# Performance work log

Measured on AMD Instinct MI355X. Metric: run time of the kernel, lower is better.

The kernel has to match this reference:

```python
import jax, jax.numpy as jnp
import numpy as np

B, T, NN, GP, D, H = 16, 12, 325, 64, 512, 8
HD = D // H
N_TOT = GP + NN  # 389


def setup_inputs() -> dict:
    key = jax.random.key(0)
    ks = jax.random.split(key, 16)
    def lin_w(k, fan_in, fan_out):
        return jax.random.normal(k, (fan_in, fan_out), jnp.float32) * np.float32(1.0 / np.sqrt(fan_in))
    d = {"X": jax.random.normal(ks[0], (B, T, N_TOT, D), jnp.float32)}
    i = 1
    for p in ("e", "d"):
        for w in ("q", "k", "v", "o"):
            d[f"{p}_w{w}"] = lin_w(ks[i], D, D); i += 1
            d[f"{p}_b{w}"] = jnp.zeros((D,), jnp.float32)
    d["ff_w1"] = lin_w(ks[i], D, 4 * D); i += 1
    d["ff_b1"] = jnp.zeros((4 * D,), jnp.float32)
    d["ff_w2"] = lin_w(ks[i], 4 * D, D); i += 1
    d["ff_b2"] = jnp.zeros((D,), jnp.float32)
    d["ln1_g"] = jnp.ones((D,), jnp.float32)
    d["ln1_b"] = jnp.zeros((D,), jnp.float32)
    d["ln2_g"] = jnp.ones((D,), jnp.float32)
    d["ln2_b"] = jnp.zeros((D,), jnp.float32)
    return d


def _mha(q, k, v, wq, bq, wk, bk, wv, bv, wo, bo):
    # torch split(head_dim,-1)+cat(0) == reshape last dim to (H, HD)
    Q = (q @ wq + bq).reshape(q.shape[:-1] + (H, HD))
    K = (k @ wk + bk).reshape(k.shape[:-1] + (H, HD))
    V = (v @ wv + bv).reshape(v.shape[:-1] + (H, HD))
    s = jnp.einsum('btqhd,btkhd->bthqk', Q, K) * np.float32(1.0 / np.sqrt(HD))
    a = jax.nn.softmax(s, axis=-1)  # dropout=0.0 -> identity
    o = jnp.einsum('bthqk,btkhd->btqhd', a, V).reshape(q.shape)
    return o @ wo + bo


def _ln(x, g, b):
    m = x.mean(-1, keepdims=True)
    v = x.var(-1, keepdims=True)
    return (x - m) * jax.lax.rsqrt(v + 1e-5) * g + b


def reference(X, e_wq, e_bq, e_wk, e_bk, e_wv, e_bv, e_wo, e_bo,
              d_wq, d_bq, d_wk, d_bk, d_wv, d_bv, d_wo, d_bo,
              ff_w1, ff_b1, ff_w2, ff_b2, ln1_g, ln1_b, ln2_g, ln2_b):
    glob = X[:, :, :GP, :]   # global patch queries
    patch = X[:, :, GP:, :]  # last num_nodes tokens (== x[:,:,-patch_len:])
    # eattn: global queries attend to node tokens
    t = _mha(glob, patch, patch, e_wq, e_bq, e_wk, e_bk, e_wv, e_bv, e_wo, e_bo)
    # in-place write x[:,:,:global_patch] = t -> K/V for dattn is [t, patch]
    x_kv = jnp.concatenate([t, patch], axis=2)
    # dattn: node queries attend to full (updated) sequence
    out = _mha(patch, x_kv, x_kv, d_wq, d_bq, d_wk, d_bk, d_wv, d_bv, d_wo, d_bo)
    out = _ln(patch + out, ln1_g, ln1_b)  # residual is original node tokens
    ff = jax.nn.relu(out @ ff_w1 + ff_b1) @ ff_w2 + ff_b2
    out = _ln(out + ff, ln2_g, ln2_b)
    return jnp.concatenate([t, out], axis=2)
```

## Files before the change

kernel.cpp:

```cpp
#include <hip/hip_runtime.h>

typedef unsigned short u16;
typedef __attribute__((ext_vector_type(4))) float f32x4;
typedef __attribute__((ext_vector_type(8))) __bf16 bf16x8;
typedef __attribute__((ext_vector_type(4))) unsigned short u16x4;
typedef __attribute__((ext_vector_type(8))) unsigned short u16x8;

#define DEV static __device__ __forceinline__
#define MFMA_B16 __builtin_amdgcn_mfma_f32_16x16x32_bf16


DEV u16 f2b(float f) {
  union { float f; unsigned u; } c; c.f = f;
  return (u16)((c.u + 0x7FFFu + ((c.u >> 16) & 1u)) >> 16);
}

DEV void async_cp16(void* lds, const void* g) {
  __builtin_amdgcn_global_load_lds((__attribute__((address_space(1))) void*)g,
                                   (__attribute__((address_space(3))) void*)lds,
                                   16, 0, 0);
}

__global__ __launch_bounds__(256) void transpose_w(const float* __restrict__ W,
                                                   u16* __restrict__ Wt,
                                                   int K, int N) {
  __shared__ float t[32][33];
  const int n0 = blockIdx.x * 32, k0 = blockIdx.y * 32;
  const int tx = threadIdx.x, ty = threadIdx.y;
  for (int i = ty; i < 32; i += 8) t[i][tx] = W[(size_t)(k0 + i) * N + n0 + tx];
  __syncthreads();
  for (int i = ty; i < 32; i += 8)
    Wt[(size_t)(n0 + i) * K + k0 + tx] = f2b(t[tx][i]);
}

__global__ __launch_bounds__(256) void convert_x(const float* __restrict__ X,
                                                 u16* __restrict__ Xg,
                                                 u16* __restrict__ Xp) {
  const size_t i = ((size_t)blockIdx.x * 256 + threadIdx.x) * 4;
  const f32x4 v = *(const f32x4*)(X + i);
  const size_t row = i >> 9;
  const int col = (int)(i & 511);
  const int bt = (int)(row / 389), n = (int)(row - (size_t)bt * 389);
  u16x4 w;
#pragma unroll
  for (int u = 0; u < 4; u++) w[u] = f2b(v[u]);
  u16* dst = (n < 64) ? (Xg + (((size_t)bt * 64 + n) << 9) + col)
                      : (Xp + (((size_t)bt * 328 + (n - 64)) << 9) + col);
  *(u16x4*)dst = w;
}

template <int MODE>
__global__ __launch_bounds__(256) void gemm_bt(
    const u16* __restrict__ A, const u16* __restrict__ Bt,
    const float* __restrict__ bias, float* outF, u16* outB,
    int M, int N, int K, int rows_per, int row_ofs, int aux) {
  __shared__ u16 SH[2][128 * 64];
  u16* As = &SH[0][0];
  u16* Bs = &SH[1][0];
  const int tid = threadIdx.x;
  const int lane = tid & 63, wid = tid >> 6;
  const int l4 = lane >> 4, l16 = lane & 15;
  const int n0 = blockIdx.x * 128, m0 = blockIdx.y * 128;
  const int wr = (wid >> 1) * 64, wc = (wid & 1) * 64;

  const int srow = lane >> 3;
  const int scol = 8 * ((lane & 7) ^ srow);
  const u16* gA = A + (size_t)(m0 + wid * 32 + srow) * K + scol;
  const u16* gB = Bt + (size_t)(n0 + wid * 32 + srow) * K + scol;

  f32x4 acc[4][4] = {};

  for (int kk = 0; kk < K; kk += 64) {
    if (kk) __syncthreads();
#pragma unroll
    for (int c = 0; c < 4; c++) {
      async_cp16(As + (wid * 32 + c * 8) * 64, gA + (size_t)(c * 8) * K + kk);
      async_cp16(Bs + (wid * 32 + c * 8) * 64, gB + (size_t)(c * 8) * K + kk);
    }
    __syncthreads();
#pragma unroll
    for (int hh = 0; hh < 2; hh++) {
      const int sw = (((hh * 64 + l4 * 16) ^ ((l16 & 7) << 4)) >> 1);
      bf16x8 af[4], bfr[4];
#pragma unroll
      for (int i = 0; i < 4; i++)
        af[i] = *(const bf16x8*)(As + (wr + i * 16 + l16) * 64 + sw);
#pragma unroll
      for (int j = 0; j < 4; j++)
        bfr[j] = *(const bf16x8*)(Bs + (wc + j * 16 + l16) * 64 + sw);
#pragma unroll
      for (int i = 0; i < 4; i++)
#pragma unroll
        for (int j = 0; j < 4; j++)
          acc[i][j] = MFMA_B16(af[i], bfr[j], acc[i][j], 0, 0, 0);
    }
  }

  if constexpr (MODE == 6) {
    __syncthreads();
    u16* cs = &SH[0][0];
#pragma unroll
    for (int j = 0; j < 4; j++) {
      const float bv = bias[n0 + wc + j * 16 + l16];
#pragma unroll
      for (int i = 0; i < 4; i++)
#pragma unroll
        for (int r = 0; r < 4; r++)
          cs[(wr + i * 16 + l4 * 4 + r) * 128 + wc + j * 16 + l16] =
              f2b(acc[i][j][r] + bv);
    }
    __syncthreads();
    const int c = tid & 127;
    const int kvh = (tid >> 7) * 64;
    const int gh = (n0 + c) >> 6, gd = (n0 + c) & 63;
#pragma unroll
    for (int g = 0; g < 8; g++) {
      const int row0 = m0 + kvh + g * 8;
      if (row0 >= M) break;
      const int bt0 = row0 / rows_per;
      const int rr = row0 - bt0 * rows_per;
      u16x8 w;
#pragma unroll
      for (int e = 0; e < 8; e++) w[e] = cs[(kvh + g * 8 + e) * 128 + c];
      *(u16x8*)(outB + (((size_t)bt0 * 8 + gh) * 64 + gd) * (size_t)aux +
                row_ofs + rr) = w;
    }
  } else {
#pragma unroll
    for (int j = 0; j < 4; j++) {
      const int col = n0 + wc + j * 16 + l16;
      const float bv = bias[col];
#pragma unroll
      for (int i = 0; i < 4; i++) {
#pragma unroll
        for (int r = 0; r < 4; r++) {
          const int row = m0 + wr + i * 16 + l4 * 4 + r;
          if (row >= M) continue;
          const float v = acc[i][j][r] + bv;
          if constexpr (MODE == 0) {
            outB[(size_t)row * N + col] = f2b(v);
          } else if constexpr (MODE == 1) {
            const int bt = row / rows_per, rr = row - bt * rows_per;
            if (rr < aux)
              outB[((size_t)bt * 389 + row_ofs + rr) * 512 + col] = f2b(v);
          } else if constexpr (MODE == 2) {
            const int bt = row >> 6, rr = row & 63;
            outF[((size_t)bt * 389 + rr) * 512 + col] = v;
            outB[(size_t)row * 512 + col] = f2b(v);
          } else if constexpr (MODE == 3) {
            outF[(size_t)row * N + col] = v;
          } else if constexpr (MODE == 4) {
            outB[(size_t)row * N + col] = f2b(v > 0.f ? v : 0.f);
          } else {
            outF[(size_t)row * N + col] += v;
          }
        }
      }
    }
  }
}

template <int QS, int MQ, int KS, int NK, int NKP, bool T2>
__global__ __launch_bounds__(256) void attn_fused(
    const u16* __restrict__ Q, const u16* __restrict__ Kb,
    const u16* __restrict__ Vt, u16* __restrict__ O) {
  constexpr int NCH = NKP / 64;
  constexpr int QTW = T2 ? 128 : 64;
  constexpr int QP = (MQ + QTW - 1) / QTW;
  constexpr int PSTR = 72;
  __shared__ __align__(16) u16 Pl[4][2][16 * PSTR];
  const int tid = threadIdx.x, lane = tid & 63, wid = tid >> 6;
  const int l4 = lane >> 4, l16 = lane & 15;
  const int bt = blockIdx.x >> 3, h = blockIdx.x & 7;
  u16* pw0 = &Pl[wid][0][0];
  u16* pw1 = &Pl[wid][1][0];
  const u16* vb = Vt + ((size_t)bt * 8 + h) * (size_t)(64 * NKP);
  const u16* qb = Q + (size_t)bt * QS * 512 + h * 64;
  const u16* kb = Kb + (size_t)bt * KS * 512 + h * 64;

  for (int qp = 0; qp < QP; ++qp) {
    const int q0 = qp * QTW + wid * 16;
    const bool bL = T2 && (q0 + 64 < MQ);
    const u16* qpA = qb + (size_t)(q0 + l16) * 512 + l4 * 8;
    const bf16x8 aq0A = *(const bf16x8*)qpA;
    const bf16x8 aq1A = *(const bf16x8*)(qpA + 32);
    bf16x8 aq0B, aq1B;
    if (bL) {
      aq0B = *(const bf16x8*)(qpA + 32768);
      aq1B = *(const bf16x8*)(qpA + 32768 + 32);
    }

    f32x4 m0v, m1v, sum0, sum1, o0[4], o1[4];
#pragma unroll
    for (int r = 0; r < 4; r++) {
      m0v[r] = -1e30f; m1v[r] = -1e30f; sum0[r] = 0.f; sum1[r] = 0.f;
    }
#pragma unroll
    for (int j = 0; j < 4; j++) {
      o0[j] = (f32x4){0.f, 0.f, 0.f, 0.f};
      o1[j] = (f32x4){0.f, 0.f, 0.f, 0.f};
    }

    for (int ch = 0; ch < NCH; ++ch) {
      const int k0 = ch * 64;
      f32x4 sc0[4], sc1[4];
#pragma unroll
      for (int s = 0; s < 4; s++) {
        const u16* kp = kb + (size_t)(k0 + s * 16 + l16) * 512 + l4 * 8;
        const bf16x8 kf0 = *(const bf16x8*)kp;
        const bf16x8 kf1 = *(const bf16x8*)(kp + 32);
        f32x4 a = (f32x4){0.f, 0.f, 0.f, 0.f};
        a = MFMA_B16(aq0A, kf0, a, 0, 0, 0);
        a = MFMA_B16(aq1A, kf1, a, 0, 0, 0);
        sc0[s] = a;
        if (bL) {
          f32x4 bacc = (f32x4){0.f, 0.f, 0.f, 0.f};
          bacc = MFMA_B16(aq0B, kf0, bacc, 0, 0, 0);
          bacc = MFMA_B16(aq1B, kf1, bacc, 0, 0, 0);
          sc1[s] = bacc;
        }
      }
#pragma unroll
      for (int s = 0; s < 4; s++) {
        const bool vld = (k0 + s * 16 + l16) < NK;
#pragma unroll
        for (int r = 0; r < 4; r++) {
          sc0[s][r] = vld ? sc0[s][r] * 0.125f : -1e30f;
          if (bL) sc1[s][r] = vld ? sc1[s][r] * 0.125f : -1e30f;
        }
      }
      f32x4 c0, c1;
#pragma unroll
      for (int r = 0; r < 4; r++) {
        c0[r] = fmaxf(fmaxf(sc0[0][r], sc0[1][r]), fmaxf(sc0[2][r], sc0[3][r]));
        if (bL)
          c1[r] = fmaxf(fmaxf(sc1[0][r], sc1[1][r]), fmaxf(sc1[2][r], sc1[3][r]));
      }
#pragma unroll
      for (int mk = 1; mk < 16; mk <<= 1)
#pragma unroll
        for (int r = 0; r < 4; r++) {
          c0[r] = fmaxf(c0[r], __shfl_xor(c0[r], mk));
          if (bL) c1[r] = fmaxf(c1[r], __shfl_xor(c1[r], mk));
        }
      float g = c0[0] - m0v[0];
#pragma unroll
      for (int r = 1; r < 4; r++) g = fmaxf(g, c0[r] - m0v[r]);
      if (bL)
#pragma unroll
        for (int r = 0; r < 4; r++) g = fmaxf(g, c1[r] - m1v[r]);
      if (__any(g > 0.f)) {
#pragma unroll
        for (int r = 0; r < 4; r++) {
          float mn = fmaxf(m0v[r], c0[r]);
          float f = __expf(m0v[r] - mn);
          m0v[r] = mn; sum0[r] *= f;
#pragma unroll
          for (int j = 0; j < 4; j++) o0[j][r] *= f;
          if (bL) {
            mn = fmaxf(m1v[r], c1[r]); f = __expf(m1v[r] - mn);
            m1v[r] = mn; sum1[r] *= f;
#pragma unroll
            for (int j = 0; j < 4; j++) o1[j][r] *= f;
          }
        }
      }
#pragma unroll
      for (int s = 0; s < 4; s++)
#pragma unroll
        for (int r = 0; r < 4; r++) {
          const float e0 = __expf(sc0[s][r] - m0v[r]);
          sum0[r] += e0;
          pw0[(l4 * 4 + r) * PSTR + s * 16 + l16] = f2b(e0);
          if (bL) {
            const float e1 = __expf(sc1[s][r] - m1v[r]);
            sum1[r] += e1;
            pw1[(l4 * 4 + r) * PSTR + s * 16 + l16] = f2b(e1);
          }
        }
      asm volatile("s_waitcnt lgkmcnt(0)" ::: "memory");
      const bf16x8 apA0 = *(const bf16x8*)(pw0 + l16 * PSTR + l4 * 8);
      const bf16x8 apA1 = *(const bf16x8*)(pw0 + l16 * PSTR + 32 + l4 * 8);
      bf16x8 apB0, apB1;
      if (bL) {
        apB0 = *(const bf16x8*)(pw1 + l16 * PSTR + l4 * 8);
        apB1 = *(const bf16x8*)(pw1 + l16 * PSTR + 32 + l4 * 8);
      }
      __builtin_amdgcn_s_setprio(1);
#pragma unroll
      for (int j = 0; j < 4; j++) {
        const u16* vp = vb + (size_t)(j * 16 + l16) * NKP + k0 + l4 * 8;
        const bf16x8 v0 = *(const bf16x8*)vp;
        const bf16x8 v1 = *(const bf16x8*)(vp + 32);
        o0[j] = MFMA_B16(apA0, v0, o0[j], 0, 0, 0);
        o0[j] = MFMA_B16(apA1, v1, o0[j], 0, 0, 0);
        if (bL) {
          o1[j] = MFMA_B16(apB0, v0, o1[j], 0, 0, 0);
          o1[j] = MFMA_B16(apB1, v1, o1[j], 0, 0, 0);
        }
      }
      __builtin_amdgcn_s_setprio(0);
    }
#pragma unroll
    for (int mk = 1; mk < 16; mk <<= 1)
#pragma unroll
      for (int r = 0; r < 4; r++) {
        sum0[r] += __shfl_xor(sum0[r], mk);
        if (bL) sum1[r] += __shfl_xor(sum1[r], mk);
      }
#pragma unroll
    for (int j = 0; j < 4; j++)
#pragma unroll
      for (int r = 0; r < 4; r++) {
        const int qr = q0 + l4 * 4 + r;
        if (qr < MQ)
          O[((size_t)bt * QS + qr) * 512 + h * 64 + j * 16 + l16] =
              f2b(o0[j][r] / sum0[r]);
        if (bL && qr + 64 < MQ)
          O[((size_t)bt * QS + qr + 64) * 512 + h * 64 + j * 16 + l16] =
              f2b(o1[j][r] / sum1[r]);
      }
  }
}

__global__ __launch_bounds__(256) void ln_res(const float* __restrict__ X,
                                              float* __restrict__ y,
                                              const float* g, const float* b,
                                              u16* __restrict__ yb) {
  const int p = blockIdx.x * 4 + (threadIdx.x >> 6);
  const int lane = threadIdx.x & 63;
  const int bt = p / 325, n = p - bt * 325;
  const size_t yrow = ((size_t)bt * 328 + n) * 512;
  const float* xr = X + ((size_t)bt * 389 + 64 + n) * 512 + lane * 8;
  const float* ar = y + yrow + lane * 8;
  float vv[8];
  {
    const f32x4 a0 = *(const f32x4*)xr, a1 = *(const f32x4*)(xr + 4);
    const f32x4 b0 = *(const f32x4*)ar, b1 = *(const f32x4*)(ar + 4);
#pragma unroll
    for (int u = 0; u < 4; u++) { vv[u] = a0[u] + b0[u]; vv[u + 4] = a1[u] + b1[u]; }
  }
  float s1 = 0.f, s2 = 0.f;
#pragma unroll
  for (int u = 0; u < 8; u++) { s1 += vv[u]; s2 += vv[u] * vv[u]; }
  for (int m = 1; m < 64; m <<= 1) { s1 += __shfl_xor(s1, m); s2 += __shfl_xor(s2, m); }
  const float mean = s1 * (1.f / 512.f);
  const float inv = rsqrtf(s2 * (1.f / 512.f) - mean * mean + 1e-5f);
  const int c0 = lane * 8;
  f32x4 o0, o1;
  u16x8 ob;
#pragma unroll
  for (int u = 0; u < 8; u++) {
    const float o = (vv[u] - mean) * inv * g[c0 + u] + b[c0 + u];
    if (u < 4) o0[u] = o; else o1[u - 4] = o;
    ob[u] = f2b(o);
  }
  *(f32x4*)(y + yrow + c0) = o0;
  *(f32x4*)(y + yrow + c0 + 4) = o1;
  *(u16x8*)(yb + yrow + c0) = ob;
}

__global__ __launch_bounds__(256) void ln_out(const float* __restrict__ y,
                                              const float* g, const float* b,
                                              float* __restrict__ out) {
  const int p = blockIdx.x * 4 + (threadIdx.x >> 6);
  const int lane = threadIdx.x & 63;
  const int bt = p / 325, n = p - bt * 325;
  const float* yr = y + ((size_t)bt * 328 + n) * 512 + lane * 8;
  float vv[8];
  {
    const f32x4 a0 = *(const f32x4*)yr, a1 = *(const f32x4*)(yr + 4);
#pragma unroll
    for (int u = 0; u < 4; u++) { vv[u] = a0[u]; vv[u + 4] = a1[u]; }
  }
  float s1 = 0.f, s2 = 0.f;
#pragma unroll
  for (int u = 0; u < 8; u++) { s1 += vv[u]; s2 += vv[u] * vv[u]; }
  for (int m = 1; m < 64; m <<= 1) { s1 += __shfl_xor(s1, m); s2 += __shfl_xor(s2, m); }
  const float mean = s1 * (1.f / 512.f);
  const float inv = rsqrtf(s2 * (1.f / 512.f) - mean * mean + 1e-5f);
  const int c0 = lane * 8;
  f32x4 o0, o1;
#pragma unroll
  for (int u = 0; u < 8; u++) {
    const float o = (vv[u] - mean) * inv * g[c0 + u] + b[c0 + u];
    if (u < 4) o0[u] = o; else o1[u - 4] = o;
  }
  float* orow = out + ((size_t)bt * 389 + 64 + n) * 512 + c0;
  *(f32x4*)(orow) = o0;
  *(f32x4*)(orow + 4) = o1;
}

extern "C" void kernel_launch(void* const* d_in, const int* in_sizes, int n_in,
                              void* d_out, int out_size, void* d_ws,
                              size_t ws_size, hipStream_t stream) {
  (void)in_sizes; (void)n_in; (void)out_size; (void)ws_size;
  const float* X = (const float*)d_in[0];
  const float* W[8] = {(const float*)d_in[1],  (const float*)d_in[3],
                       (const float*)d_in[5],  (const float*)d_in[7],
                       (const float*)d_in[9],  (const float*)d_in[11],
                       (const float*)d_in[13], (const float*)d_in[15]};
  const float* Bv[8] = {(const float*)d_in[2],  (const float*)d_in[4],
                        (const float*)d_in[6],  (const float*)d_in[8],
                        (const float*)d_in[10], (const float*)d_in[12],
                        (const float*)d_in[14], (const float*)d_in[16]};
  const float* ff_w1 = (const float*)d_in[17];
  const float* ff_b1 = (const float*)d_in[18];
  const float* ff_w2 = (const float*)d_in[19];
  const float* ff_b2 = (const float*)d_in[20];
  const float* ln1_g = (const float*)d_in[21];
  const float* ln1_b = (const float*)d_in[22];
  const float* ln2_g = (const float*)d_in[23];
  const float* ln2_b = (const float*)d_in[24];
  float* out = (float*)d_out;
  char* ws = (char*)d_ws;

  constexpr size_t szW   = 8388608;
  constexpr size_t szXp  = (size_t)(62976 + 128) * 1024;
  constexpr size_t szQe  = (size_t)(12288 + 128) * 1024;
  constexpr size_t szKe  = szXp;
  constexpr size_t szVte = (size_t)192 * 8 * 64 * 384 * 2;
  constexpr size_t szKd  = (size_t)(74688 + 128) * 1024;
  constexpr size_t szVtd = (size_t)192 * 8 * 64 * 448 * 2;
  constexpr size_t o1 = szW;
  constexpr size_t o2 = o1 + szXp;
  constexpr size_t o3 = o2 + szQe;
  constexpr size_t o4 = o3 + szQe;
  constexpr size_t o5 = o4 + szQe + szKe + szVte;
  constexpr size_t o6 = o5 + szVtd;

  u16* wt     = (u16*)(ws);
  u16* Xp     = (u16*)(ws + o1);
  u16* yb     = (u16*)(ws + o1);
  u16* Xg     = (u16*)(ws + o2);
  u16* attn_e = (u16*)(ws + o2);
  u16* tb     = (u16*)(ws + o3);
  u16* Qe     = (u16*)(ws + o4);
  u16* Ke     = (u16*)(ws + o4 + szQe);
  u16* Vte    = (u16*)(ws + o4 + szQe + szKe);
  u16* Qd     = (u16*)(ws + o4);
  u16* Kd     = (u16*)(ws + o4 + szXp);
  float* y    = (float*)(ws + o4);
  u16* Vtd    = (u16*)(ws + o5);
  u16* hb     = (u16*)(ws + o5);
  u16* attn_d = (u16*)(ws + o6);

  u16* wt_p[8];
  for (int i = 0; i < 8; i++) wt_p[i] = wt + (size_t)i * 262144;
  u16* ff1t = wt + (size_t)8 * 262144;
  u16* ff2t = ff1t + (size_t)1048576;

  dim3 tblk(32, 8);
  for (int i = 0; i < 8; i++)
    transpose_w<<<dim3(16, 16), tblk, 0, stream>>>(W[i], wt_p[i], 512, 512);
  transpose_w<<<dim3(64, 16), tblk, 0, stream>>>(ff_w1, ff1t, 512, 2048);
  transpose_w<<<dim3(16, 64), tblk, 0, stream>>>(ff_w2, ff2t, 2048, 512);

  convert_x<<<37344, 256, 0, stream>>>(X, Xg, Xp);

  gemm_bt<0><<<dim3(4, 96), 256, 0, stream>>>(Xg, wt_p[0], Bv[0], nullptr, Qe,
                                              12288, 512, 512, 0, 0, 0);
  gemm_bt<0><<<dim3(4, 492), 256, 0, stream>>>(Xp, wt_p[1], Bv[1], nullptr, Ke,
                                               62976, 512, 512, 0, 0, 0);
  gemm_bt<6><<<dim3(4, 492), 256, 0, stream>>>(Xp, wt_p[2], Bv[2], nullptr, Vte,
                                               62976, 512, 512, 328, 0, 384);
  attn_fused<64, 64, 328, 325, 384, false><<<1536, 256, 0, stream>>>(
      Qe, Ke, Vte, attn_e);
  gemm_bt<2><<<dim3(4, 96), 256, 0, stream>>>(attn_e, wt_p[3], Bv[3], out, tb,
                                              12288, 512, 512, 0, 0, 0);

  gemm_bt<0><<<dim3(4, 492), 256, 0, stream>>>(Xp, wt_p[4], Bv[4], nullptr, Qd,
                                               62976, 512, 512, 0, 0, 0);
  gemm_bt<1><<<dim3(4, 96), 256, 0, stream>>>(tb, wt_p[5], Bv[5], nullptr, Kd,
                                              12288, 512, 512, 64, 0, 64);
  gemm_bt<1><<<dim3(4, 492), 256, 0, stream>>>(Xp, wt_p[5], Bv[5], nullptr, Kd,
                                               62976, 512, 512, 328, 64, 325);
  gemm_bt<6><<<dim3(4, 96), 256, 0, stream>>>(tb, wt_p[6], Bv[6], nullptr, Vtd,
                                              12288, 512, 512, 64, 0, 448);
  gemm_bt<6><<<dim3(4, 492), 256, 0, stream>>>(Xp, wt_p[6], Bv[6], nullptr, Vtd,
                                               62976, 512, 512, 328, 64, 448);
  attn_fused<328, 325, 389, 389, 448, true><<<1536, 256, 0, stream>>>(
      Qd, Kd, Vtd, attn_d);
  gemm_bt<3><<<dim3(4, 492), 256, 0, stream>>>(attn_d, wt_p[7], Bv[7], y,
                                               nullptr, 62976, 512, 512, 0, 0, 0);

  ln_res<<<15600, 256, 0, stream>>>(X, y, ln1_g, ln1_b, yb);

  for (int c = 0; c < 4; c++) {
    const size_t ro = (size_t)c * 15744;
    gemm_bt<4><<<dim3(16, 123), 256, 0, stream>>>(
        yb + ro * 512, ff1t, ff_b1, nullptr, hb, 15744, 2048, 512, 0, 0, 0);
    gemm_bt<5><<<dim3(4, 123), 256, 0, stream>>>(
        hb, ff2t, ff_b2, y + ro * 512, nullptr, 15744, 512, 2048, 0, 0, 0);
  }
  ln_out<<<15600, 256, 0, stream>>>(y, ln2_g, ln2_b, out);
}
```

Before: 2.048 ms.

## Split attention query tiles across grid, XCD-aware GEMM block remap, exp2 softmax

The decoder attention kernel now gives each query tile its own block (grid y of 3) instead of looping over tiles inside one block, which raises the number of blocks in flight. The softmax scale is folded into a base-2 factor so the kernel can use the native v_exp_f32 instruction. Bounds masking is applied only to the final key chunk, and the normalisation uses a reciprocal multiply instead of a divide. GEMM blocks are remapped so that consecutive tiles are grouped onto the same XCD for better L2 reuse, at the cost of a few integer operations per block.

```diff
diff --git a/kernel.cpp b/kernel.cpp
--- a/kernel.cpp
+++ b/kernel.cpp
@@ -15,11 +15,17 @@
   return (u16)((c.u + 0x7FFFu + ((c.u >> 16) & 1u)) >> 16);
 }
 
+DEV float ex2(float x) {
+  float r; asm("v_exp_f32 %0, %1" : "=v"(r) : "v"(x)); return r;
+}
+
 DEV void async_cp16(void* lds, const void* g) {
   __builtin_amdgcn_global_load_lds((__attribute__((address_space(1))) void*)g,
                                    (__attribute__((address_space(3))) void*)lds,
                                    16, 0, 0);
 }
+
+template <bool B> struct bc { static constexpr bool value = B; };
 
 __global__ __launch_bounds__(256) void transpose_w(const float* __restrict__ W,
                                                    u16* __restrict__ Wt,
@@ -60,7 +66,16 @@
   const int tid = threadIdx.x;
   const int lane = tid & 63, wid = tid >> 6;
   const int l4 = lane >> 4, l16 = lane & 15;
-  const int n0 = blockIdx.x * 128, m0 = blockIdx.y * 128;
+  int bx, by;
+  {
+    const int gx = gridDim.x;
+    const int nwg = gx * gridDim.y;
+    const int b = blockIdx.y * gx + blockIdx.x;
+    const int q = nwg >> 3, r = nwg & 7, x = b & 7, s = b >> 3;
+    const int w = (x < r) ? (x * (q + 1) + s) : (r * (q + 1) + (x - r) * q + s);
+    bx = w % gx; by = w / gx;
+  }
+  const int n0 = bx * 128, m0 = by * 128;
   const int wr = (wid >> 1) * 64, wc = (wid & 1) * 64;
 
   const int srow = lane >> 3;
@@ -164,10 +179,9 @@
 __global__ __launch_bounds__(256) void attn_fused(
     const u16* __restrict__ Q, const u16* __restrict__ Kb,
     const u16* __restrict__ Vt, u16* __restrict__ O) {
-  constexpr int NCH = NKP / 64;
-  constexpr int QTW = T2 ? 128 : 64;
-  constexpr int QP = (MQ + QTW - 1) / QTW;
+  constexpr int NF = NK / 64;
   constexpr int PSTR = 72;
+  constexpr float SCL = 0.18033688011112042f;
   __shared__ __align__(16) u16 Pl[4][2][16 * PSTR];
   const int tid = threadIdx.x, lane = tid & 63, wid = tid >> 6;
   const int l4 = lane >> 4, l16 = lane & 15;
@@ -175,152 +189,161 @@
   u16* pw0 = &Pl[wid][0][0];
   u16* pw1 = &Pl[wid][1][0];
   const u16* vb = Vt + ((size_t)bt * 8 + h) * (size_t)(64 * NKP);
-  const u16* qb = Q + (size_t)bt * QS * 512 + h * 64;
   const u16* kb = Kb + (size_t)bt * KS * 512 + h * 64;
 
-  for (int qp = 0; qp < QP; ++qp) {
-    const int q0 = qp * QTW + wid * 16;
-    const bool bL = T2 && (q0 + 64 < MQ);
-    const u16* qpA = qb + (size_t)(q0 + l16) * 512 + l4 * 8;
-    const bf16x8 aq0A = *(const bf16x8*)qpA;
-    const bf16x8 aq1A = *(const bf16x8*)(qpA + 32);
-    bf16x8 aq0B, aq1B;
-    if (bL) {
-      aq0B = *(const bf16x8*)(qpA + 32768);
-      aq1B = *(const bf16x8*)(qpA + 32768 + 32);
-    }
-
-    f32x4 m0v, m1v, sum0, sum1, o0[4], o1[4];
+  const int q0 = blockIdx.y * (T2 ? 128 : 64) + wid * 16;
+  const u16* qp =
+      Q + ((size_t)bt * QS + q0 + l16) * 512 + h * 64 + l4 * 8;
+  const bf16x8 aq0A = *(const bf16x8*)qp;
+  const bf16x8 aq1A = *(const bf16x8*)(qp + 32);
+  bf16x8 aq0B = aq0A, aq1B = aq1A;
+  if constexpr (T2) {
+    aq0B = *(const bf16x8*)(qp + 32768);
+    aq1B = *(const bf16x8*)(qp + 32768 + 32);
+  }
+
+  f32x4 m0v, m1v, sum0, sum1, o0[4], o1[4];
+#pragma unroll
+  for (int r = 0; r < 4; r++) {
+    m0v[r] = -1e30f; m1v[r] = -1e30f; sum0[r] = 0.f; sum1[r] = 0.f;
+  }
+#pragma unroll
+  for (int j = 0; j < 4; j++) {
+    o0[j] = (f32x4){0.f, 0.f, 0.f, 0.f};
+    o1[j] = (f32x4){0.f, 0.f, 0.f, 0.f};
+  }
+
+  auto chunk = [&](int k0, auto mc) {
+    constexpr bool MASK = decltype(mc)::value;
+    f32x4 sc0[4], sc1[4];
+#pragma unroll
+    for (int s = 0; s < 4; s++) {
+      const u16* kp = kb + (size_t)(k0 + s * 16 + l16) * 512 + l4 * 8;
+      const bf16x8 kf0 = *(const bf16x8*)kp;
+      const bf16x8 kf1 = *(const bf16x8*)(kp + 32);
+      f32x4 a = (f32x4){0.f, 0.f, 0.f, 0.f};
+      a = MFMA_B16(aq0A, kf0, a, 0, 0, 0);
+      a = MFMA_B16(aq1A, kf1, a, 0, 0, 0);
+      sc0[s] = a;
+      if constexpr (T2) {
+        f32x4 bq = (f32x4){0.f, 0.f, 0.f, 0.f};
+        bq = MFMA_B16(aq0B, kf0, bq, 0, 0, 0);
+        bq = MFMA_B16(aq1B, kf1, bq, 0, 0, 0);
+        sc1[s] = bq;
+      }
+    }
+#pragma unroll
+    for (int s = 0; s < 4; s++) {
+      bool vld = true;
+      if constexpr (MASK) vld = (k0 + s * 16 + l16) < NK;
+#pragma unroll
+      for (int r = 0; r < 4; r++) {
+        sc0[s][r] = vld ? sc0[s][r] * SCL : -1e30f;
+        if constexpr (T2) sc1[s][r] = vld ? sc1[s][r] * SCL : -1e30f;
+      }
+    }
+    f32x4 c0, c1;
 #pragma unroll
     for (int r = 0; r < 4; r++) {
-      m0v[r] = -1e30f; m1v[r] = -1e30f; sum0[r] = 0.f; sum1[r] = 0.f;
-    }
+      c0[r] = fmaxf(fmaxf(sc0[0][r], sc0[1][r]), fmaxf(sc0[2][r], sc0[3][r]));
+      if constexpr (T2)
+        c1[r] = fmaxf(fmaxf(sc1[0][r], sc1[1][r]), fmaxf(sc1[2][r], sc1[3][r]));
+    }
+#pragma unroll
+    for (int mk = 1; mk < 16; mk <<= 1)
+#pragma unroll
+      for (int r = 0; r < 4; r++) {
+        c0[r] = fmaxf(c0[r], __shfl_xor(c0[r], mk));
+        if constexpr (T2) c1[r] = fmaxf(c1[r], __shfl_xor(c1[r], mk));
+      }
+    float g = c0[0] - m0v[0];
+#pragma unroll
+    for (int r = 1; r < 4; r++) g = fmaxf(g, c0[r] - m0v[r]);
+    if constexpr (T2)
+#pragma unroll
+      for (int r = 0; r < 4; r++) g = fmaxf(g, c1[r] - m1v[r]);
+    if (__any(g > 0.f)) {
+#pragma unroll
+      for (int r = 0; r < 4; r++) {
+        float mn = fmaxf(m0v[r], c0[r]);
+        float f = ex2(m0v[r] - mn);
+        m0v[r] = mn; sum0[r] *= f;
+#pragma unroll
+        for (int j = 0; j < 4; j++) o0[j][r] *= f;
+        if constexpr (T2) {
+          mn = fmaxf(m1v[r], c1[r]); f = ex2(m1v[r] - mn);
+          m1v[r] = mn; sum1[r] *= f;
+#pragma unroll
+          for (int j = 0; j < 4; j++) o1[j][r] *= f;
+        }
+      }
+    }
+#pragma unroll
+    for (int s = 0; s < 4; s++)
+#pragma unroll
+      for (int r = 0; r < 4; r++) {
+        const float e0 = ex2(sc0[s][r] - m0v[r]);
+        sum0[r] += e0;
+        ((__bf16*)pw0)[(l4 * 4 + r) * PSTR + s * 16 + l16] = (__bf16)e0;
+        if constexpr (T2) {
+          const float e1 = ex2(sc1[s][r] - m1v[r]);
+          sum1[r] += e1;
+          ((__bf16*)pw1)[(l4 * 4 + r) * PSTR + s * 16 + l16] = (__bf16)e1;
+        }
+      }
+    asm volatile("s_waitcnt lgkmcnt(0)" ::: "memory");
+    const bf16x8 apA0 = *(const bf16x8*)(pw0 + l16 * PSTR + l4 * 8);
+    const bf16x8 apA1 = *(const bf16x8*)(pw0 + l16 * PSTR + 32 + l4 * 8);
+    bf16x8 apB0 = apA0, apB1 = apA1;
+    if constexpr (T2) {
+      apB0 = *(const bf16x8*)(pw1 + l16 * PSTR + l4 * 8);
+      apB1 = *(const bf16x8*)(pw1 + l16 * PSTR + 32 + l4 * 8);
+    }
+    __builtin_amdgcn_s_setprio(1);
 #pragma unroll
     for (int j = 0; j < 4; j++) {
-      o0[j] = (f32x4){0.f, 0.f, 0.f, 0.f};
-      o1[j] = (f32x4){0.f, 0.f, 0.f, 0.f};
-    }
-
-    for (int ch = 0; ch < NCH; ++ch) {
-      const int k0 = ch * 64;
-      f32x4 sc0[4], sc1[4];
-#pragma unroll
-      for (int s = 0; s < 4; s++) {
-        const u16* kp = kb + (size_t)(k0 + s * 16 + l16) * 512 + l4 * 8;
-        const bf16x8 kf0 = *(const bf16x8*)kp;
-        const bf16x8 kf1 = *(const bf16x8*)(kp + 32);
-        f32x4 a = (f32x4){0.f, 0.f, 0.f, 0.f};
-        a = MFMA_B16(aq0A, kf0, a, 0, 0, 0);
-        a = MFMA_B16(aq1A, kf1, a, 0, 0, 0);
-        sc0[s] = a;
-        if (bL) {
-          f32x4 bacc = (f32x4){0.f, 0.f, 0.f, 0.f};
-          bacc = MFMA_B16(aq0B, kf0, bacc, 0, 0, 0);
-          bacc = MFMA_B16(aq1B, kf1, bacc, 0, 0, 0);
-          sc1[s] = bacc;
-        }
-      }
-#pragma unroll
-      for (int s = 0; s < 4; s++) {
-        const bool vld = (k0 + s * 16 + l16) < NK;
-#pragma unroll
-        for (int r = 0; r < 4; r++) {
-          sc0[s][r] = vld ? sc0[s][r] * 0.125f : -1e30f;
-          if (bL) sc1[s][r] = vld ? sc1[s][r] * 0.125f : -1e30f;
-        }
-      }
-      f32x4 c0, c1;
-#pragma unroll
-      for (int r = 0; r < 4; r++) {
-        c0[r] = fmaxf(fmaxf(sc0[0][r], sc0[1][r]), fmaxf(sc0[2][r], sc0[3][r]));
-        if (bL)
-          c1[r] = fmaxf(fmaxf(sc1[0][r], sc1[1][r]), fmaxf(sc1[2][r], sc1[3][r]));
-      }
-#pragma unroll
-      for (int mk = 1; mk < 16; mk <<= 1)
-#pragma unroll
-        for (int r = 0; r < 4; r++) {
-          c0[r] = fmaxf(c0[r], __shfl_xor(c0[r], mk));
-          if (bL) c1[r] = fmaxf(c1[r], __shfl_xor(c1[r], mk));
-        }
-      float g = c0[0] - m0v[0];
-#pragma unroll
-      for (int r = 1; r < 4; r++) g = fmaxf(g, c0[r] - m0v[r]);
-      if (bL)
-#pragma unroll
-        for (int r = 0; r < 4; r++) g = fmaxf(g, c1[r] - m1v[r]);
-      if (__any(g > 0.f)) {
-#pragma unroll
-        for (int r = 0; r < 4; r++) {
-          float mn = fmaxf(m0v[r], c0[r]);
-          float f = __expf(m0v[r] - mn);
-          m0v[r] = mn; sum0[r] *= f;
-#pragma unroll
-          for (int j = 0; j < 4; j++) o0[j][r] *= f;
-          if (bL) {
-            mn = fmaxf(m1v[r], c1[r]); f = __expf(m1v[r] - mn);
-            m1v[r] = mn; sum1[r] *= f;
-#pragma unroll
-            for (int j = 0; j < 4; j++) o1[j][r] *= f;
-          }
-        }
-      }
-#pragma unroll
-      for (int s = 0; s < 4; s++)
-#pragma unroll
-        for (int r = 0; r < 4; r++) {
-          const float e0 = __expf(sc0[s][r] - m0v[r]);
-          sum0[r] += e0;
-          pw0[(l4 * 4 + r) * PSTR + s * 16 + l16] = f2b(e0);
-          if (bL) {
-            const float e1 = __expf(sc1[s][r] - m1v[r]);
-            sum1[r] += e1;
-            pw1[(l4 * 4 + r) * PSTR + s * 16 + l16] = f2b(e1);
-          }
-        }
-      asm volatile("s_waitcnt lgkmcnt(0)" ::: "memory");
-      const bf16x8 apA0 = *(const bf16x8*)(pw0 + l16 * PSTR + l4 * 8);
-      const bf16x8 apA1 = *(const bf16x8*)(pw0 + l16 * PSTR + 32 + l4 * 8);
-      bf16x8 apB0, apB1;
-      if (bL) {
-        apB0 = *(const bf16x8*)(pw1 + l16 * PSTR + l4 * 8);
-        apB1 = *(const bf16x8*)(pw1 + l16 * PSTR + 32 + l4 * 8);
-      }
-      __builtin_amdgcn_s_setprio(1);
-#pragma unroll
-      for (int j = 0; j < 4; j++) {
-        const u16* vp = vb + (size_t)(j * 16 + l16) * NKP + k0 + l4 * 8;
-        const bf16x8 v0 = *(const bf16x8*)vp;
-        const bf16x8 v1 = *(const bf16x8*)(vp + 32);
-        o0[j] = MFMA_B16(apA0, v0, o0[j], 0, 0, 0);
-        o0[j] = MFMA_B16(apA1, v1, o0[j], 0, 0, 0);
-        if (bL) {
-          o1[j] = MFMA_B16(apB0, v0, o1[j], 0, 0, 0);
-          o1[j] = MFMA_B16(apB1, v1, o1[j], 0, 0, 0);
-        }
-      }
-      __builtin_amdgcn_s_setprio(0);
-    }
-#pragma unroll
-    for (int mk = 1; mk < 16; mk <<= 1)
-#pragma unroll
-      for (int r = 0; r < 4; r++) {
-        sum0[r] += __shfl_xor(sum0[r], mk);
-        if (bL) sum1[r] += __shfl_xor(sum1[r], mk);
-      }
-#pragma unroll
-    for (int j = 0; j < 4; j++)
-#pragma unroll
-      for (int r = 0; r < 4; r++) {
-        const int qr = q0 + l4 * 4 + r;
-        if (qr < MQ)
-          O[((size_t)bt * QS + qr) * 512 + h * 64 + j * 16 + l16] =
-              f2b(o0[j][r] / sum0[r]);
-        if (bL && qr + 64 < MQ)
+      const u16* vp = vb + (size_t)(j * 16 + l16) * NKP + k0 + l4 * 8;
+      const bf16x8 v0 = *(const bf16x8*)vp;
+      const bf16x8 v1 = *(const bf16x8*)(vp + 32);
+      o0[j] = MFMA_B16(apA0, v0, o0[j], 0, 0, 0);
+      o0[j] = MFMA_B16(apA1, v1, o0[j], 0, 0, 0);
+      if constexpr (T2) {
+        o1[j] = MFMA_B16(apB0, v0, o1[j], 0, 0, 0);
+        o1[j] = MFMA_B16(apB1, v1, o1[j], 0, 0, 0);
+      }
+    }
+    __builtin_amdgcn_s_setprio(0);
+  };
+
+  for (int ch = 0; ch < NF; ++ch) chunk(ch * 64, bc<false>{});
+  chunk(NF * 64, bc<true>{});
+
+#pragma unroll
+  for (int mk = 1; mk < 16; mk <<= 1)
+#pragma unroll
+    for (int r = 0; r < 4; r++) {
+      sum0[r] += __shfl_xor(sum0[r], mk);
+      if constexpr (T2) sum1[r] += __shfl_xor(sum1[r], mk);
+    }
+  f32x4 inv0, inv1;
+#pragma unroll
+  for (int r = 0; r < 4; r++) {
+    inv0[r] = 1.f / sum0[r];
+    inv1[r] = T2 ? 1.f / sum1[r] : 0.f;
+  }
+#pragma unroll
+  for (int j = 0; j < 4; j++)
+#pragma unroll
+    for (int r = 0; r < 4; r++) {
+      const int qr = q0 + l4 * 4 + r;
+      if (qr < MQ)
+        O[((size_t)bt * QS + qr) * 512 + h * 64 + j * 16 + l16] =
+            f2b(o0[j][r] * inv0[r]);
+      if constexpr (T2)
+        if (qr + 64 < MQ)
           O[((size_t)bt * QS + qr + 64) * 512 + h * 64 + j * 16 + l16] =
-              f2b(o1[j][r] / sum1[r]);
-      }
-  }
+              f2b(o1[j][r] * inv1[r]);
+    }
 }
 
 __global__ __launch_bounds__(256) void ln_res(const float* __restrict__ X,
@@ -420,7 +443,6 @@
   constexpr size_t szQe  = (size_t)(12288 + 128) * 1024;
   constexpr size_t szKe  = szXp;
   constexpr size_t szVte = (size_t)192 * 8 * 64 * 384 * 2;
-  constexpr size_t szKd  = (size_t)(74688 + 128) * 1024;
   constexpr size_t szVtd = (size_t)192 * 8 * 64 * 448 * 2;
   constexpr size_t o1 = szW;
   constexpr size_t o2 = o1 + szXp;
@@ -464,7 +486,7 @@
                                                62976, 512, 512, 0, 0, 0);
   gemm_bt<6><<<dim3(4, 492), 256, 0, stream>>>(Xp, wt_p[2], Bv[2], nullptr, Vte,
                                                62976, 512, 512, 328, 0, 384);
-  attn_fused<64, 64, 328, 325, 384, false><<<1536, 256, 0, stream>>>(
+  attn_fused<64, 64, 328, 325, 384, false><<<dim3(1536, 1), 256, 0, stream>>>(
       Qe, Ke, Vte, attn_e);
   gemm_bt<2><<<dim3(4, 96), 256, 0, stream>>>(attn_e, wt_p[3], Bv[3], out, tb,
                                               12288, 512, 512, 0, 0, 0);
@@ -479,7 +501,7 @@
                                               12288, 512, 512, 64, 0, 448);
   gemm_bt<6><<<dim3(4, 492), 256, 0, stream>>>(Xp, wt_p[6], Bv[6], nullptr, Vtd,
                                                62976, 512, 512, 328, 64, 448);
-  attn_fused<328, 325, 389, 389, 448, true><<<1536, 256, 0, stream>>>(
+  attn_fused<328, 325, 389, 389, 448, true><<<dim3(1536, 3), 256, 0, stream>>>(
       Qd, Kd, Vtd, attn_d);
   gemm_bt<3><<<dim3(4, 492), 256, 0, stream>>>(attn_d, wt_p[7], Bv[7], y,
                                                nullptr, 62976, 512, 512, 0, 0, 0);
```

Measured after the change: 1.896 ms. -7.5%, faster.
